# Performance work log

Measured on AMD Instinct MI355X. Metric: run time of the kernel, lower is better.

## Reference

```python
import jax, jax.numpy as jnp
import numpy as np
import math

D = 128
RATIO = 0.8
BN_EPS = 1e-5
N_NODES = 40000
N_EDGES = 640000
Y_SIZE = 8


def _prelu(x, a):
    return jnp.where(x > 0, x, a * x)


def setup_inputs() -> dict:
    key = jax.random.key(0)
    ks = jax.random.split(key, 16)
    inv = lambda n: 1.0 / np.sqrt(n)
    return {
        "x": jax.random.normal(ks[0], (N_NODES, 1), jnp.float32),
        "edge_index": jax.random.randint(ks[1], (2, N_EDGES), 0, N_NODES, jnp.int32),
        "W1": jax.random.normal(ks[2], (1, D), jnp.float32),
        "V1": jax.random.normal(ks[3], (1, D), jnp.float32),
        "Ws": jax.random.normal(ks[4], (9, D, D), jnp.float32) * inv(D),
        "Vs": jax.random.normal(ks[5], (9, D, D), jnp.float32) * inv(D),
        "conv_b": jax.random.normal(ks[6], (10, D), jnp.float32) * 0.01,
        "bn_gamma": 1.0 + 0.1 * jax.random.normal(ks[7], (10, D), jnp.float32),
        "bn_beta": 0.1 * jax.random.normal(ks[8], (10, D), jnp.float32),
        "bn_mean": jnp.zeros((10, D), jnp.float32),
        "bn_var": jnp.ones((10, D), jnp.float32),
        "pool_p": jax.random.normal(ks[9], (10, D), jnp.float32),
        "prelu_a": 0.25 * jnp.ones((1,), jnp.float32),
        "lin1_w": jax.random.normal(ks[10], (2560, 1280), jnp.float32) * inv(2560),
        "lin1_b": jax.random.normal(ks[11], (1280,), jnp.float32) * 0.01,
        "lin2_w": jax.random.normal(ks[12], (1280, Y_SIZE), jnp.float32) * inv(1280),
        "lin2_b": jax.random.normal(ks[13], (Y_SIZE,), jnp.float32) * 0.01,
    }


def reference(x, edge_index, W1, V1, Ws, Vs, conv_b, bn_gamma, bn_beta, bn_mean,
              bn_var, pool_p, prelu_a, lin1_w, lin1_b, lin2_w, lin2_b):
    # Single graph (batch all zeros). Edge array stays fixed size with a validity mask.
    src, dst = edge_index[0], edge_index[1]
    emask = jnp.ones(src.shape, dtype=bool)
    n = x.shape[0]
    h = x
    reads = []
    for i in range(10):
        W = W1 if i == 0 else Ws[i - 1]
        V = V1 if i == 0 else Vs[i - 1]
        # ---- ARMAConv (num_stacks=1, num_layers=1): relu(L_hat (h W) + h V + b)
        ew = emask.astype(h.dtype)
        deg = jax.ops.segment_sum(ew, dst, num_segments=n)
        dinv = jnp.where(deg > 0, 1.0 / jnp.sqrt(deg), 0.0)
        norm = dinv[dst] * dinv[src] * ew                      # [E]
        hw = h @ W                                             # [n, D]
        agg = jax.ops.segment_sum(hw[src] * norm[:, None], dst, num_segments=n)
        h = jax.nn.relu(agg + h @ V + conv_b[i])
        # ---- BatchNorm1d (eval mode, running stats)
        h = (h - bn_mean[i]) * (bn_gamma[i] / jnp.sqrt(bn_var[i] + BN_EPS)) + bn_beta[i]
        # ---- shared PReLU
        h = _prelu(h, prelu_a)
        # ---- TopKPooling(ratio=0.8): score = tanh(h.p/||p||), keep ceil(0.8n)
        p = pool_p[i]
        score = jnp.tanh(h @ p / jnp.linalg.norm(p))
        k = math.ceil(RATIO * n)
        topv, idx = jax.lax.top_k(score, k)
        h = h[idx] * topv[:, None]                             # [k, D]
        remap = jnp.full((n,), -1, jnp.int32).at[idx].set(jnp.arange(k, dtype=jnp.int32))
        ns, nd = remap[src], remap[dst]
        emask = emask & (ns >= 0) & (nd >= 0)
        src = jnp.where(emask, ns, 0)
        dst = jnp.where(emask, nd, 0)
        n = k
        # ---- global max + mean pool (single graph)
        reads.append(jnp.concatenate([h.max(axis=0), h.mean(axis=0)]))
    r = jnp.concatenate(reads)[None, :]                        # [1, 2560]
    z = _prelu(r @ lin1_w + lin1_b, prelu_a)                   # dropout = identity (eval)
    z = _prelu(z @ lin2_w + lin2_b, prelu_a)
    z = z - z.min(axis=1, keepdims=True)
    z = z / z.max(axis=1, keepdims=True)
    z = z / z.sum(axis=1, keepdims=True)
    return z
```

## Files before the change

kernel.cpp:

```cpp
#include <hip/hip_runtime.h>
#include <hip/hip_bf16.h>

#define NEDGE 640000
#define NMAX  40000
#define SB    40
#define PRB   256
#define EBLK  512
#define FB    1280
#define LIN1B 64
#define GRB   32
#define HTS   36
#define TKB   32
#define GHN   5632
#define GBMAX 2048

__device__ inline unsigned orderKey(float s) {
    unsigned b = __float_as_uint(s);
    return (b & 0x80000000u) ? ~b : (b | 0x80000000u);
}

__device__ inline void histAdd(int* sh, int bin, bool act, int nbits) {
    unsigned long long mm = __ballot(act);
    for (int b = 0; b < nbits; b++) {
        unsigned long long bal = __ballot(act && ((bin >> b) & 1));
        mm &= ((bin >> b) & 1) ? bal : ~bal;
    }
    if (act) {
        int lane = threadIdx.x & 63;
        int leader = __ffsll(mm) - 1;
        if (lane == leader) atomicAdd(&sh[bin], __popcll(mm));
    }
}

__device__ inline void gridbar(int* ctr, int target) {
    __syncthreads();
    if (threadIdx.x == 0) {
        __threadfence();
        __hip_atomic_fetch_add(ctr, 1, __ATOMIC_RELEASE, __HIP_MEMORY_SCOPE_AGENT);
        while (__hip_atomic_load(ctr, __ATOMIC_ACQUIRE, __HIP_MEMORY_SCOPE_AGENT) < target)
            __builtin_amdgcn_s_sleep(1);
        __threadfence();
    }
    __syncthreads();
}

__device__ inline void suffixSel2048(int* lh, const int* gh, int rem, int* outD, int* outR) {
    int t = threadIdx.x;
    lh[t] = gh[t]; lh[t+1024] = gh[t+1024];
    __syncthreads();
    for (int off = 1; off < 2048; off <<= 1) {
        int v0 = lh[t]      + ((t+off < 2048)      ? lh[t+off]      : 0);
        int v1 = lh[t+1024] + ((t+1024+off < 2048) ? lh[t+1024+off] : 0);
        __syncthreads();
        lh[t] = v0; lh[t+1024] = v1;
        __syncthreads();
    }
    for (int d = t; d < 2048; d += 1024) {
        int S = lh[d], Sn = (d == 2047) ? 0 : lh[d+1];
        if (S >= rem && Sn < rem) { *outD = d; *outR = rem - Sn; }
    }
    __syncthreads();
}

__device__ inline void suffixSel1024(int* lh, const int* gh, int rem, int* outD, int* outR) {
    int t = threadIdx.x;
    lh[t] = gh[t];
    __syncthreads();
    for (int off = 1; off < 1024; off <<= 1) {
        int v0 = lh[t] + ((t+off < 1024) ? lh[t+off] : 0);
        __syncthreads();
        lh[t] = v0;
        __syncthreads();
    }
    {
        int S = lh[t], Sn = (t == 1023) ? 0 : lh[t+1];
        if (S >= rem && Sn < rem) { *outD = t; *outR = rem - Sn; }
    }
    __syncthreads();
}

__device__ inline void prefixSel256(int* lh, const int* gh, int rem, int* outD, int* outR) {
    int t = threadIdx.x;
    if (t < 256) lh[t] = gh[t];
    __syncthreads();
    for (int off = 1; off < 256; off <<= 1) {
        int v = 0;
        if (t < 256) v = lh[t] + ((t >= off) ? lh[t-off] : 0);
        __syncthreads();
        if (t < 256) lh[t] = v;
        __syncthreads();
    }
    if (t < 256) {
        int P = lh[t], Pp = (t == 0) ? 0 : lh[t-1];
        if (P >= rem && Pp < rem) { *outD = t; *outR = rem - Pp; }
    }
    __syncthreads();
}

__device__ inline void poolReduceT(const float* __restrict__ scr, float* __restrict__ rbuf,
                                   int gbP, int L, int ch) {
    int t = threadIdx.x;
    bool isMax = ch < 128;
    float acc = isMax ? -3.402823e38f : 0.f;
    for (int r = t; r < gbP; r += 256) {
        float v = scr[(size_t)ch*GBMAX + r];
        acc = isMax ? fmaxf(acc, v) : (acc + v);
    }
    __shared__ float red[256];
    red[t] = acc; __syncthreads();
    for (int st = 128; st > 0; st >>= 1) {
        if (t < st) red[t] = isMax ? fmaxf(red[t], red[t+st]) : (red[t] + red[t+st]);
        __syncthreads();
    }
    if (t == 0) rbuf[L*256 + ch] = red[0];
}

__device__ const float c_invk[10] = {
    1.0f/32000.0f, 1.0f/25600.0f, 1.0f/20480.0f, 1.0f/16384.0f, 1.0f/13108.0f,
    1.0f/10487.0f, 1.0f/8390.0f,  1.0f/6712.0f,  1.0f/5370.0f,  1.0f/4296.0f };

__global__ void k_init(const int* __restrict__ eidx, int* __restrict__ esrc,
                       int* __restrict__ edst, int* __restrict__ erank,
                       const float* __restrict__ poolp,
                       float* __restrict__ rbuf, float* __restrict__ pnorm,
                       int* __restrict__ ecnt, int* __restrict__ degA,
                       int* __restrict__ tkc) {
    int b = blockIdx.x, t = threadIdx.x;
    if (b < 10) {
        rbuf[b*256 + t] = (t < 128) ? -3.402823e38f : 0.0f;
        __shared__ float red[256];
        float v = 0.0f;
        if (t < 128) { float pv = poolp[b*128 + t]; v = pv*pv; }
        red[t] = v; __syncthreads();
        for (int s = 128; s > 0; s >>= 1) { if (t < s) red[t] += red[t+s]; __syncthreads(); }
        if (t == 0) pnorm[b] = sqrtf(red[0]);
    }
    if (b == 10 && t < 16) ecnt[t] = (t == 0) ? NEDGE : 0;
    if (b == 11 && t < 64) tkc[t] = 0;
    int e = b*256 + t;
    if (e < NEDGE) {
        int d = eidx[NEDGE + e];
        esrc[e] = eidx[e]; edst[e] = d;
        erank[e] = atomicAdd(&degA[d], 1);
    }
}

__global__ __launch_bounds__(256) void k_presum(const int* __restrict__ deg,
                                                int* __restrict__ lbsum,
                                                int n, int chunk) {
    int b = blockIdx.x, t = threadIdx.x;
    __shared__ int red[256];
    int start = b*chunk, end = min(start + chunk, n);
    int s = 0;
    for (int i = start + t; i < end; i += 256) s += deg[i];
    red[t] = s; __syncthreads();
    for (int st = 128; st > 0; st >>= 1) { if (t < st) red[t] += red[t+st]; __syncthreads(); }
    if (t == 0) lbsum[b] = red[0];
}

__global__ void k_scan(const int* __restrict__ deg,
                       int* __restrict__ offs, float* __restrict__ dinv,
                       int* __restrict__ ghist, int* __restrict__ selbuf,
                       const int* __restrict__ lbsum,
                       const float* __restrict__ scr, float* __restrict__ rbuf,
                       int n, int chunk, int gbP, int prevL) {
    int b = blockIdx.x, t = threadIdx.x, lane = t & 63, wid = t >> 6;
    if (b >= SB) {
        if (gbP > 0) poolReduceT(scr, rbuf, gbP, prevL, b - SB);
        return;
    }
    __shared__ int s_excl;
    __shared__ int wsum[4];
    __shared__ int s_carry;
    __shared__ int s_sums[SB];
    if (b == 0) {
        for (int jj = t; jj < GHN; jj += 256) ghist[jj] = 0;
        if (t == 0) { selbuf[2] = 0; selbuf[5] = 0; }
    }
    if (t < SB) s_sums[t] = lbsum[t];
    __syncthreads();
    if (t == 0) {
        int excl = 0;
        for (int p = 0; p < b; p++) excl += s_sums[p];
        s_excl = excl;
    }
    __syncthreads();
    if (t == 0) s_carry = s_excl;
    __syncthreads();
    int start = b*chunk, end = min(start + chunk, n);
    for (int base = start; base < end; base += 256) {
        int i = base + t;
        int d = (i < end) ? deg[i] : 0;
        int incl = d;
        for (int off = 1; off < 64; off <<= 1) {
            int o = __shfl_up(incl, off);
            if (lane >= off) incl += o;
        }
        if (lane == 63) wsum[wid] = incl;
        __syncthreads();
        if (t == 0) { int c = s_carry; for (int w = 0; w < 4; w++) { int tmp = wsum[w]; wsum[w] = c; c += tmp; } s_carry = c; }
        __syncthreads();
        int p = wsum[wid] + incl - d;
        if (i < end) {
            offs[i] = p;
            dinv[i] = (d > 0) ? 1.0f/sqrtf((float)d) : 0.0f;
        }
        __syncthreads();
    }
}

__global__ __launch_bounds__(128) void k_fill(const int* __restrict__ esrc, const int* __restrict__ edst,
                                              const int* __restrict__ erank, const int* __restrict__ offs,
                                              int* __restrict__ csr, const int* __restrict__ ecnt) {
    int ec = *ecnt;
    for (int e = blockIdx.x*128 + threadIdx.x; e < ec; e += FB*128)
        csr[offs[edst[e]] + erank[e]] = esrc[e];
}

__global__ __launch_bounds__(128) void k_gather0(
    const float* __restrict__ x, const float* __restrict__ W1, const float* __restrict__ V1,
    const float* __restrict__ convb,
    const float* __restrict__ bng, const float* __restrict__ bnb,
    const float* __restrict__ bnm, const float* __restrict__ bnv,
    const float* __restrict__ poolp, const float* __restrict__ pnorm,
    const float* __restrict__ prelua,
    const int* __restrict__ offs, const int* __restrict__ deg, const float* __restrict__ dinv,
    const int* __restrict__ csr,
    float* __restrict__ AGG, float* __restrict__ score, unsigned* __restrict__ keys) {
    int v = blockIdx.x, j = threadIdx.x;
    __shared__ float red[128];
    int off = offs[v], dg = deg[v];
    float accs = 0.0f;
    for (int c = j; c < dg; c += 128) { int s = csr[off + c]; accs += x[s]*dinv[s]; }
    red[j] = accs; __syncthreads();
    for (int st = 64; st > 0; st >>= 1) { if (j < st) red[j] += red[j+st]; __syncthreads(); }
    float aggs = red[0] * dinv[v];
    __syncthreads();
    float h2 = aggs*W1[j] + x[v]*V1[j] + convb[j];
    h2 = fmaxf(h2, 0.0f);
    float scale = bng[j] / sqrtf(bnv[j] + 1e-5f);
    h2 = (h2 - bnm[j])*scale + bnb[j];
    float a = prelua[0];
    h2 = (h2 > 0.0f) ? h2 : a*h2;
    AGG[v*128 + j] = h2;
    red[j] = h2 * poolp[j]; __syncthreads();
    for (int st = 64; st > 0; st >>= 1) { if (j < st) red[j] += red[j+st]; __syncthreads(); }
    if (j == 0) {
        float sc = tanhf(red[0] / pnorm[0]);
        score[v] = sc;
        keys[v]  = orderKey(sc);
    }
}

__global__ __launch_bounds__(128) void k_gather(
    const float* __restrict__ HW, float* __restrict__ AGG,
    const int* __restrict__ offs, const int* __restrict__ deg, const float* __restrict__ dinv,
    const int* __restrict__ csr,
    const float* __restrict__ bng, const float* __restrict__ bnb,
    const float* __restrict__ bnm, const float* __restrict__ bnv,
    const float* __restrict__ poolp, const float* __restrict__ pnorm,
    const float* __restrict__ prelua,
    float* __restrict__ score, unsigned* __restrict__ keys, int layer) {
    int v = blockIdx.x, j = threadIdx.x;
    __shared__ int   s_src[128];
    __shared__ float s_dv[128];
    __shared__ float red[128];
    int off = offs[v], dg = deg[v];
    float acc = 0.0f;
    for (int base = 0; base < dg; base += 128) {
        int cnt = min(128, dg - base);
        if (j < cnt) { int s = csr[off + base + j]; s_src[j] = s; s_dv[j] = dinv[s]; }
        __syncthreads();
        for (int c = 0; c < cnt; c++) acc += HW[s_src[c]*128 + j] * s_dv[c];
        __syncthreads();
    }
    int gj = layer*128 + j;
    float h2 = AGG[v*128 + j] + acc*dinv[v];
    h2 = fmaxf(h2, 0.0f);
    float scale = bng[gj] / sqrtf(bnv[gj] + 1e-5f);
    h2 = (h2 - bnm[gj])*scale + bnb[gj];
    float a = prelua[0];
    h2 = (h2 > 0.0f) ? h2 : a*h2;
    AGG[v*128 + j] = h2;
    red[j] = h2 * poolp[gj]; __syncthreads();
    for (int st = 64; st > 0; st >>= 1) { if (j < st) red[j] += red[j+st]; __syncthreads(); }
    if (j == 0) {
        float sc = tanhf(red[0] / pnorm[layer]);
        score[v] = sc;
        keys[v]  = orderKey(sc);
    }
}

__global__ __launch_bounds__(1024) void k_topk(const unsigned* __restrict__ keys,
                                               int* __restrict__ gh, int* __restrict__ selbuf,
                                               int* __restrict__ degN,
                                               int* __restrict__ remap, int* __restrict__ keep_ids,
                                               int* __restrict__ bar, int n, int kk) {
    __shared__ int lh[2048];
    __shared__ int s_d1, s_r1, s_dA, s_rA, s_dB, s_ntk, s_bC, s_r2, s_lowD, s_lowR;
    __shared__ int s_base, s_cur;
    int t = threadIdx.x, b = blockIdx.x, lane = t & 63;
    int* h1 = gh;
    int* h2 = gh + 2048;
    int* h3 = gh + 4096;
    int* h4 = gh + 5120;
    int* h5 = gh + 5376;

    for (int i = b*1024 + t; i < NMAX; i += TKB*1024) degN[i] = 0;

    int nR = (n + 1023) & ~1023;
    lh[t] = 0; lh[t+1024] = 0;
    __syncthreads();
    for (int i = b*1024 + t; i < nR; i += TKB*1024) {
        bool act = (i < n);
        int bin = act ? (int)(keys[i] >> 21) : 0;
        histAdd(lh, bin, act, 11);
    }
    __syncthreads();
    { int c = lh[t]; if (c) atomicAdd(&h1[t], c); c = lh[t+1024]; if (c) atomicAdd(&h1[t+1024], c); }
    gridbar(&bar[0], TKB);
    suffixSel2048(lh, h1, kk, &s_d1, &s_r1);
    int bstar = s_d1;

    lh[t] = 0; lh[t+1024] = 0;
    __syncthreads();
    for (int i = b*1024 + t; i < nR; i += TKB*1024) {
        bool act = false; int bin = 0;
        if (i < n) { unsigned key = keys[i]; act = ((int)(key >> 21) == bstar); bin = (int)((key >> 10) & 2047); }
        histAdd(lh, act ? bin : 0, act, 11);
    }
    __syncthreads();
    { int c = lh[t]; if (c) atomicAdd(&h2[t], c); c = lh[t+1024]; if (c) atomicAdd(&h2[t+1024], c); }
    gridbar(&bar[1], TKB);
    suffixSel2048(lh, h2, s_r1, &s_dA, &s_rA);
    unsigned top21 = ((unsigned)bstar << 11) | (unsigned)s_dA;

    lh[t] = 0;
    __syncthreads();
    for (int i = b*1024 + t; i < nR; i += TKB*1024) {
        bool act = false; int bin = 0;
        if (i < n) { unsigned key = keys[i]; act = ((key >> 10) == top21); bin = (int)(key & 1023); }
        histAdd(lh, act ? bin : 0, act, 10);
    }
    __syncthreads();
    { int c = lh[t]; if (c) atomicAdd(&h3[t], c); }
    gridbar(&bar[2], TKB);
    suffixSel1024(lh, h3, s_rA, &s_dB, &s_ntk);
    unsigned thresh = (top21 << 10) | (unsigned)s_dB;

    if (t < 256) lh[t] = 0;
    __syncthreads();
    for (int i = b*1024 + t; i < n; i += TKB*1024)
        if (keys[i] == thresh) atomicAdd(&lh[i >> 8], 1);
    __syncthreads();
    if (t < 256) { int c = lh[t]; if (c) atomicAdd(&h4[t], c); }
    gridbar(&bar[3], TKB);
    prefixSel256(lh, h4, s_ntk, &s_bC, &s_r2);
    int bC = s_bC;

    if (t < 256) lh[t] = 0;
    __syncthreads();
    for (int i = b*1024 + t; i < n; i += TKB*1024)
        if (keys[i] == thresh && (i >> 8) == bC) atomicAdd(&lh[i & 255], 1);
    __syncthreads();
    if (t < 256) { int c = lh[t]; if (c) atomicAdd(&h5[t], c); }
    gridbar(&bar[4], TKB);
    prefixSel256(lh, h5, s_r2, &s_lowD, &s_lowR);
    int cut = (bC << 8) | s_lowD;

    {
        int cnt = 0;
        for (int base = b*1024; base < n; base += TKB*1024) {
            int i = base + t;
            if (i < n) {
                unsigned key = keys[i];
                cnt += (key > thresh) || (key == thresh && i <= cut);
            }
        }
        lh[t] = cnt; __syncthreads();
        for (int st = 512; st > 0; st >>= 1) { if (t < st) lh[t] += lh[t+st]; __syncthreads(); }
        if (t == 0) { s_base = atomicAdd(&selbuf[5], lh[0]); s_cur = 0; }
        __syncthreads();
        for (int base = b*1024; base < n; base += TKB*1024) {
            int i = base + t;
            bool keep = false;
            if (i < n) {
                unsigned key = keys[i];
                keep = (key > thresh) || (key == thresh && i <= cut);
            }
            unsigned long long m = __ballot(keep);
            int wcnt = __popcll(m);
            int wbase = 0;
            if (lane == 0 && wcnt) wbase = atomicAdd(&s_cur, wcnt);
            wbase = __shfl(wbase, 0);
            if (keep) {
                int slot = s_base + wbase + __popcll(m & ((1ULL << lane) - 1));
                remap[i] = slot; keep_ids[slot] = i;
            } else if (i < n) remap[i] = -1;
        }
    }
}

__global__ __launch_bounds__(128) void k_poolgemm(
        const float* __restrict__ AGGc, const float* __restrict__ score,
        const int* __restrict__ keep_ids, const int* __restrict__ remap,
        float* __restrict__ scr,
        const int* __restrict__ esrcP, const int* __restrict__ edstP,
        int* __restrict__ esrcN, int* __restrict__ edstN, int* __restrict__ erankN,
        const int* __restrict__ ecntP, int* __restrict__ ecntN, int* __restrict__ degN,
        const float* __restrict__ W, const float* __restrict__ V, const float* __restrict__ bias,
        float* __restrict__ HW, float* __restrict__ AGGn, int k, int gb, int do_gemm) {
    int b = blockIdx.x, t = threadIdx.x;
    __shared__ __align__(16) float ht[128*HTS];
    if (b < gb) {
        int v0 = b * GRB;
        float mx = -3.402823e38f, sm = 0.f;
        #pragma unroll
        for (int it = 0; it < GRB; it++) {
            int r = v0 + it;
            bool valid = (r < k);
            int vv = keep_ids[valid ? r : (k - 1)];
            float val = AGGc[(size_t)vv*128 + t] * score[vv];
            if (!valid) val = 0.f;
            ht[t*HTS + it] = val;
            if (valid) { mx = fmaxf(mx, val); sm += val; }
        }
        scr[(size_t)t*GBMAX + b]         = mx;
        scr[(size_t)(t+128)*GBMAX + b]   = sm;
        if (!do_gemm) return;
        __syncthreads();
        float accW[GRB], accV[GRB];
        #pragma unroll
        for (int r = 0; r < GRB; r++) { accW[r] = 0.0f; accV[r] = 0.0f; }
        #pragma unroll 4
        for (int kk = 0; kk < 128; kk++) {
            float mw = W[kk*128 + t];
            float mv = V[kk*128 + t];
            const float* hp = &ht[kk*HTS];
            #pragma unroll
            for (int r4 = 0; r4 < GRB; r4 += 4) {
                float4 hq = *(const float4*)(hp + r4);
                accW[r4+0] += hq.x*mw;  accV[r4+0] += hq.x*mv;
                accW[r4+1] += hq.y*mw;  accV[r4+1] += hq.y*mv;
                accW[r4+2] += hq.z*mw;  accV[r4+2] += hq.z*mv;
                accW[r4+3] += hq.w*mw;  accV[r4+3] += hq.w*mv;
            }
        }
        float bb = bias[t];
        for (int r = 0; r < GRB; r++) {
            int v = v0 + r;
            if (v >= k) break;
            HW[(size_t)v*128 + t]   = accW[r];
            AGGn[(size_t)v*128 + t] = accV[r] + bb;
        }
    } else {
        int eb = b - gb, lane = t & 63;
        int ec = *ecntP;
        int* red = (int*)ht;
        __shared__ int s_base, s_cur;
        int cnt = 0;
        for (int base = eb*128; base < ec; base += EBLK*128) {
            int e = base + t;
            if (e < ec) {
                int ns = remap[esrcP[e]], nd = remap[edstP[e]];
                cnt += (ns >= 0 && nd >= 0);
            }
        }
        red[t] = cnt; __syncthreads();
        for (int st = 64; st > 0; st >>= 1) { if (t < st) red[t] += red[t+st]; __syncthreads(); }
        if (t == 0) { s_base = atomicAdd(ecntN, red[0]); s_cur = 0; }
        __syncthreads();
        for (int base = eb*128; base < ec; base += EBLK*128) {
            int e = base + t;
            bool keep = false; int ns = 0, nd = 0;
            if (e < ec) {
                ns = remap[esrcP[e]]; nd = remap[edstP[e]];
                keep = (ns >= 0 && nd >= 0);
            }
            unsigned long long m = __ballot(keep);
            int wcnt = __popcll(m);
            int wbase = 0;
            if (lane == 0 && wcnt) wbase = atomicAdd(&s_cur, wcnt);
            wbase = __shfl(wbase, 0);
            if (keep) {
                int pos = s_base + wbase + __popcll(m & ((1ULL << lane) - 1));
                esrcN[pos] = ns; edstN[pos] = nd;
                erankN[pos] = atomicAdd(&degN[nd], 1);
            }
        }
    }
}

__global__ __launch_bounds__(256) void k_pred(const float* __restrict__ scr, float* __restrict__ rbuf,
                                              int gbP, int L) {
    poolReduceT(scr, rbuf, gbP, L, blockIdx.x);
}

__global__ __launch_bounds__(320) void k_lin1(const float* __restrict__ rbuf,
                                              const float* __restrict__ w1,
                                              float* __restrict__ z1part) {
    int b = blockIdx.x, t = threadIdx.x;
    int j = t*4;
    float4 acc = make_float4(0.f, 0.f, 0.f, 0.f);
    int i0 = b*40;
    for (int r = 0; r < 40; r++) {
        int i = i0 + r;
        float rv = rbuf[i];
        if (i & 128) rv *= c_invk[i >> 8];
        float4 w = *(const float4*)(w1 + (size_t)i*1280 + j);
        acc.x += rv*w.x; acc.y += rv*w.y; acc.z += rv*w.z; acc.w += rv*w.w;
    }
    *(float4*)(z1part + b*1280 + j) = acc;
}

__global__ __launch_bounds__(320) void k_lin2(const float* __restrict__ z1part,
                                              const float* __restrict__ b1,
                                              const float* __restrict__ w2, const float* __restrict__ b2,
                                              const float* __restrict__ prelua, float* __restrict__ out) {
    int t = threadIdx.x, lane = t & 63, wid = t >> 6;
    float a = prelua[0];
    int j = t*4;
    float4 acc = make_float4(0.f, 0.f, 0.f, 0.f);
    for (int p = 0; p < LIN1B; p++) {
        float4 v = *(const float4*)(z1part + p*1280 + j);
        acc.x += v.x; acc.y += v.y; acc.z += v.z; acc.w += v.w;
    }
    float4 bb = *(const float4*)(b1 + j);
    float z0 = acc.x + bb.x; z0 = z0 > 0.f ? z0 : a*z0;
    float z1 = acc.y + bb.y; z1 = z1 > 0.f ? z1 : a*z1;
    float z2 = acc.z + bb.z; z2 = z2 > 0.f ? z2 : a*z2;
    float z3 = acc.w + bb.w; z3 = z3 > 0.f ? z3 : a*z3;
    float s[8];
    #pragma unroll
    for (int o = 0; o < 8; o++)
        s[o] = z0*w2[(j+0)*8+o] + z1*w2[(j+1)*8+o] + z2*w2[(j+2)*8+o] + z3*w2[(j+3)*8+o];
    #pragma unroll
    for (int off = 32; off > 0; off >>= 1)
        #pragma unroll
        for (int o = 0; o < 8; o++) s[o] += __shfl_down(s[o], off);
    __shared__ float sred[5][8];
    if (lane == 0)
        for (int o = 0; o < 8; o++) sred[wid][o] = s[o];
    __syncthreads();
    if (t == 0) {
        float zo[8];
        for (int o = 0; o < 8; o++) {
            float z = sred[0][o]+sred[1][o]+sred[2][o]+sred[3][o]+sred[4][o] + b2[o];
            zo[o] = z > 0.f ? z : a*z;
        }
        float mn = zo[0];
        for (int o = 1; o < 8; o++) mn = fminf(mn, zo[o]);
        float v[8], mx = -3.402823e38f;
        for (int o = 0; o < 8; o++) { v[o] = zo[o] - mn; mx = fmaxf(mx, v[o]); }
        float sm = 0.f;
        for (int o = 0; o < 8; o++) { v[o] = v[o] / mx; sm += v[o]; }
        for (int o = 0; o < 8; o++) out[o] = v[o] / sm;
    }
}

extern "C" void kernel_launch(void* const* d_in, const int* in_sizes, int n_in,
                              void* d_out, int out_size, void* d_ws, size_t ws_size,
                              hipStream_t stream) {
    const float* x      = (const float*)d_in[0];
    const int*   eidx   = (const int*)  d_in[1];
    const float* W1     = (const float*)d_in[2];
    const float* V1     = (const float*)d_in[3];
    const float* Ws     = (const float*)d_in[4];
    const float* Vs     = (const float*)d_in[5];
    const float* convb  = (const float*)d_in[6];
    const float* bng    = (const float*)d_in[7];
    const float* bnb    = (const float*)d_in[8];
    const float* bnm    = (const float*)d_in[9];
    const float* bnv    = (const float*)d_in[10];
    const float* poolp  = (const float*)d_in[11];
    const float* prelua = (const float*)d_in[12];
    const float* w1     = (const float*)d_in[13];
    const float* b1     = (const float*)d_in[14];
    const float* w2     = (const float*)d_in[15];
    const float* b2     = (const float*)d_in[16];
    float* out = (float*)d_out;

    float* wsf  = (float*)d_ws;
    float* aggA   = wsf;
    float* aggB   = aggA  + (size_t)NMAX*128;
    float* HW     = aggB  + (size_t)NMAX*128;
    float* dinv   = HW    + (size_t)NMAX*128;
    float* score  = dinv  + NMAX;
    float* rbuf   = score + NMAX;
    float* pnorm  = rbuf  + 2560;
    float* z1part = pnorm + 16;
    float* scr    = z1part + LIN1B*1280;
    unsigned* keys = (unsigned*)(scr + (size_t)GBMAX*256);
    int* esrcA  = (int*)(keys + NMAX);
    int* edstA  = esrcA + NEDGE;
    int* erankA = edstA + NEDGE;
    int* esrcB  = erankA + NEDGE;
    int* edstB  = esrcB + NEDGE;
    int* erankB = edstB + NEDGE;
    int* csr    = erankB + NEDGE;
    int* degA   = csr   + NEDGE;
    int* degB   = degA  + NMAX;
    int* ghist  = degB  + NMAX;
    int* offs   = ghist + GHN;
    int* remap  = offs  + NMAX;
    int* keep_ids = remap + NMAX;
    int* lbsum  = keep_ids + NMAX;
    int* ecnt   = lbsum + SB*2;
    int* selbuf = ecnt  + 16;
    int* tkc    = selbuf + 16;

    static const int NS[10] = {40000,32000,25600,20480,16384,13108,10487,8390,6712,5370};
    static const int KS[10] = {32000,25600,20480,16384,13108,10487,8390,6712,5370,4296};

    hipMemsetAsync(degA, 0, (size_t)NMAX*sizeof(int), stream);
    k_init<<<2500, 256, 0, stream>>>(eidx, esrcA, edstA, erankA, poolp, rbuf, pnorm,
                                     ecnt, degA, tkc);

    for (int i = 0; i < 10; i++) {
        int n = NS[i], k = KS[i];
        int chunk = (n + SB - 1) / SB;
        int* esrcP  = (i & 1) ? esrcB  : esrcA;
        int* edstP  = (i & 1) ? edstB  : edstA;
        int* erankP = (i & 1) ? erankB : erankA;
        int* esrcN  = (i & 1) ? esrcA  : esrcB;
        int* edstN  = (i & 1) ? edstA  : edstB;
        int* erankN = (i & 1) ? erankA : erankB;
        int* degP   = (i & 1) ? degB : degA;
        int* degN   = (i & 1) ? degA : degB;
        float* AGGc = (i & 1) ? aggB : aggA;
        float* AGGn = (i & 1) ? aggA : aggB;

        int gbP = (i == 0) ? 0 : (KS[i-1] + GRB - 1) / GRB;
        k_presum<<<SB, 256, 0, stream>>>(degP, lbsum, n, chunk);
        k_scan<<<SB + PRB, 256, 0, stream>>>(degP, offs, dinv, ghist, selbuf,
                                             lbsum, scr, rbuf, n, chunk,
                                             gbP, i - 1);

        k_fill<<<FB, 128, 0, stream>>>(esrcP, edstP, erankP, offs, csr, &ecnt[i]);

        if (i == 0) {
            k_gather0<<<n, 128, 0, stream>>>(x, W1, V1, convb,
                                             bng, bnb, bnm, bnv, poolp, pnorm, prelua,
                                             offs, degP, dinv, csr, AGGc, score, keys);
        } else {
            k_gather<<<n, 128, 0, stream>>>(HW, AGGc, offs, degP, dinv, csr,
                                            bng, bnb, bnm, bnv, poolp, pnorm, prelua,
                                            score, keys, i);
        }

        k_topk<<<TKB, 1024, 0, stream>>>(keys, ghist, selbuf, degN,
                                         remap, keep_ids, tkc + i*5, n, k);

        int gb = (k + GRB - 1) / GRB;
        int do_gemm = (i < 9);
        int grid = gb + (do_gemm ? EBLK : 0);
        k_poolgemm<<<grid, 128, 0, stream>>>(AGGc, score, keep_ids, remap, scr,
                                             esrcP, edstP, esrcN, edstN, erankN,
                                             &ecnt[i], &ecnt[i+1], degN,
                                             Ws + (size_t)min(i,8)*16384,
                                             Vs + (size_t)min(i,8)*16384,
                                             convb + min(i+1,9)*128,
                                             HW, AGGn, k, gb, do_gemm);
    }

    k_pred<<<PRB, 256, 0, stream>>>(scr, rbuf, (KS[9] + GRB - 1) / GRB, 9);
    k_lin1<<<LIN1B, 320, 0, stream>>>(rbuf, w1, z1part);
    k_lin2<<<1, 320, 0, stream>>>(z1part, b1, w2, b2, prelua, out);
}
```

Measured before the change: 1.179 ms.

## Speed up top-k selection scans, skip tie-break passes, and shrink GEMM row tile

```diff
diff --git a/kernel.cpp b/kernel.cpp
--- a/kernel.cpp
+++ b/kernel.cpp
@@ -8,8 +8,8 @@
 #define EBLK  512
 #define FB    1280
 #define LIN1B 64
-#define GRB   32
-#define HTS   36
+#define GRB   16
+#define HTS   20
 #define TKB   32
 #define GHN   5632
 #define GBMAX 2048
@@ -44,38 +44,63 @@
     __syncthreads();
 }
 
-__device__ inline void suffixSel2048(int* lh, const int* gh, int rem, int* outD, int* outR) {
-    int t = threadIdx.x;
-    lh[t] = gh[t]; lh[t+1024] = gh[t+1024];
-    __syncthreads();
-    for (int off = 1; off < 2048; off <<= 1) {
-        int v0 = lh[t]      + ((t+off < 2048)      ? lh[t+off]      : 0);
-        int v1 = lh[t+1024] + ((t+1024+off < 2048) ? lh[t+1024+off] : 0);
-        __syncthreads();
-        lh[t] = v0; lh[t+1024] = v1;
-        __syncthreads();
-    }
-    for (int d = t; d < 2048; d += 1024) {
-        int S = lh[d], Sn = (d == 2047) ? 0 : lh[d+1];
-        if (S >= rem && Sn < rem) { *outD = d; *outR = rem - Sn; }
-    }
-    __syncthreads();
-}
-
-__device__ inline void suffixSel1024(int* lh, const int* gh, int rem, int* outD, int* outR) {
-    int t = threadIdx.x;
-    lh[t] = gh[t];
-    __syncthreads();
-    for (int off = 1; off < 1024; off <<= 1) {
-        int v0 = lh[t] + ((t+off < 1024) ? lh[t+off] : 0);
-        __syncthreads();
-        lh[t] = v0;
-        __syncthreads();
-    }
-    {
-        int S = lh[t], Sn = (t == 1023) ? 0 : lh[t+1];
-        if (S >= rem && Sn < rem) { *outD = t; *outR = rem - Sn; }
-    }
+__device__ inline int waveScanIncl(int v) {
+    int lane = threadIdx.x & 63;
+    #pragma unroll
+    for (int off = 1; off < 64; off <<= 1) {
+        int o = __shfl_up(v, off);
+        if (lane >= off) v += o;
+    }
+    return v;
+}
+
+__device__ inline void selScan2048(const int* gh, int rem, int* outD, int* outR, int* outCnt) {
+    __shared__ int wtot[16];
+    __shared__ int s_T;
+    int t = threadIdx.x, lane = t & 63, wid = t >> 6;
+    int a0 = gh[2*t], a1 = gh[2*t+1];
+    int s  = a0 + a1;
+    int ws = waveScanIncl(s);
+    if (lane == 63) wtot[wid] = ws;
+    __syncthreads();
+    if (t < 16) {
+        int v = wtot[t];
+        #pragma unroll
+        for (int off = 1; off < 16; off <<= 1) { int o = __shfl_up(v, off); if (lane >= off) v += o; }
+        wtot[t] = v;
+        if (t == 15) s_T = v;
+    }
+    __syncthreads();
+    int base = (wid > 0) ? wtot[wid-1] : 0;
+    int inclPair = base + ws;
+    int P1 = inclPair - a1;
+    int P0 = P1 - a0;
+    int Q = s_T - rem;
+    if (a0 > 0 && P0 <= Q && Q < P0 + a0) { *outD = 2*t;   *outR = a0 - (Q - P0); *outCnt = a0; }
+    if (a1 > 0 && P1 <= Q && Q < P1 + a1) { *outD = 2*t+1; *outR = a1 - (Q - P1); *outCnt = a1; }
+    __syncthreads();
+}
+
+__device__ inline void selScan1024(const int* gh, int rem, int* outD, int* outR, int* outCnt) {
+    __shared__ int wtot[16];
+    __shared__ int s_T;
+    int t = threadIdx.x, lane = t & 63, wid = t >> 6;
+    int a0 = gh[t];
+    int ws = waveScanIncl(a0);
+    if (lane == 63) wtot[wid] = ws;
+    __syncthreads();
+    if (t < 16) {
+        int v = wtot[t];
+        #pragma unroll
+        for (int off = 1; off < 16; off <<= 1) { int o = __shfl_up(v, off); if (lane >= off) v += o; }
+        wtot[t] = v;
+        if (t == 15) s_T = v;
+    }
+    __syncthreads();
+    int base = (wid > 0) ? wtot[wid-1] : 0;
+    int P0 = base + ws - a0;
+    int Q = s_T - rem;
+    if (a0 > 0 && P0 <= Q && Q < P0 + a0) { *outD = t; *outR = a0 - (Q - P0); *outCnt = a0; }
     __syncthreads();
 }
 
@@ -297,7 +322,7 @@
                                                int* __restrict__ remap, int* __restrict__ keep_ids,
                                                int* __restrict__ bar, int n, int kk) {
     __shared__ int lh[2048];
-    __shared__ int s_d1, s_r1, s_dA, s_rA, s_dB, s_ntk, s_bC, s_r2, s_lowD, s_lowR;
+    __shared__ int s_d1, s_r1, s_c1, s_dA, s_rA, s_cA, s_dB, s_ntk, s_cnt3, s_bC, s_r2, s_lowD, s_lowR;
     __shared__ int s_base, s_cur;
     int t = threadIdx.x, b = blockIdx.x, lane = t & 63;
     int* h1 = gh;
@@ -319,7 +344,7 @@
     __syncthreads();
     { int c = lh[t]; if (c) atomicAdd(&h1[t], c); c = lh[t+1024]; if (c) atomicAdd(&h1[t+1024], c); }
     gridbar(&bar[0], TKB);
-    suffixSel2048(lh, h1, kk, &s_d1, &s_r1);
+    selScan2048(h1, kk, &s_d1, &s_r1, &s_c1);
     int bstar = s_d1;
 
     lh[t] = 0; lh[t+1024] = 0;
@@ -332,7 +357,7 @@
     __syncthreads();
     { int c = lh[t]; if (c) atomicAdd(&h2[t], c); c = lh[t+1024]; if (c) atomicAdd(&h2[t+1024], c); }
     gridbar(&bar[1], TKB);
-    suffixSel2048(lh, h2, s_r1, &s_dA, &s_rA);
+    selScan2048(h2, s_r1, &s_dA, &s_rA, &s_cA);
     unsigned top21 = ((unsigned)bstar << 11) | (unsigned)s_dA;
 
     lh[t] = 0;
@@ -345,28 +370,33 @@
     __syncthreads();
     { int c = lh[t]; if (c) atomicAdd(&h3[t], c); }
     gridbar(&bar[2], TKB);
-    suffixSel1024(lh, h3, s_rA, &s_dB, &s_ntk);
+    selScan1024(h3, s_rA, &s_dB, &s_ntk, &s_cnt3);
     unsigned thresh = (top21 << 10) | (unsigned)s_dB;
 
-    if (t < 256) lh[t] = 0;
-    __syncthreads();
-    for (int i = b*1024 + t; i < n; i += TKB*1024)
-        if (keys[i] == thresh) atomicAdd(&lh[i >> 8], 1);
-    __syncthreads();
-    if (t < 256) { int c = lh[t]; if (c) atomicAdd(&h4[t], c); }
-    gridbar(&bar[3], TKB);
-    prefixSel256(lh, h4, s_ntk, &s_bC, &s_r2);
-    int bC = s_bC;
-
-    if (t < 256) lh[t] = 0;
-    __syncthreads();
-    for (int i = b*1024 + t; i < n; i += TKB*1024)
-        if (keys[i] == thresh && (i >> 8) == bC) atomicAdd(&lh[i & 255], 1);
-    __syncthreads();
-    if (t < 256) { int c = lh[t]; if (c) atomicAdd(&h5[t], c); }
-    gridbar(&bar[4], TKB);
-    prefixSel256(lh, h5, s_r2, &s_lowD, &s_lowR);
-    int cut = (bC << 8) | s_lowD;
+    int cut;
+    if (s_cnt3 == s_ntk) {
+        cut = n - 1;
+    } else {
+        if (t < 256) lh[t] = 0;
+        __syncthreads();
+        for (int i = b*1024 + t; i < n; i += TKB*1024)
+            if (keys[i] == thresh) atomicAdd(&lh[i >> 8], 1);
+        __syncthreads();
+        if (t < 256) { int c = lh[t]; if (c) atomicAdd(&h4[t], c); }
+        gridbar(&bar[3], TKB);
+        prefixSel256(lh, h4, s_ntk, &s_bC, &s_r2);
+        int bC = s_bC;
+
+        if (t < 256) lh[t] = 0;
+        __syncthreads();
+        for (int i = b*1024 + t; i < n; i += TKB*1024)
+            if (keys[i] == thresh && (i >> 8) == bC) atomicAdd(&lh[i & 255], 1);
+        __syncthreads();
+        if (t < 256) { int c = lh[t]; if (c) atomicAdd(&h5[t], c); }
+        gridbar(&bar[4], TKB);
+        prefixSel256(lh, h5, s_r2, &s_lowD, &s_lowR);
+        cut = (bC << 8) | s_lowD;
+    }
 
     {
         int cnt = 0;
@@ -425,28 +455,72 @@
             ht[t*HTS + it] = val;
             if (valid) { mx = fmaxf(mx, val); sm += val; }
         }
-        scr[(size_t)t*GBMAX + b]         = mx;
-        scr[(size_t)(t+128)*GBMAX + b]   = sm;
+        scr[(size_t)t*GBMAX + b]       = mx;
+        scr[(size_t)(t+128)*GBMAX + b] = sm;
         if (!do_gemm) return;
         __syncthreads();
         float accW[GRB], accV[GRB];
         #pragma unroll
         for (int r = 0; r < GRB; r++) { accW[r] = 0.0f; accV[r] = 0.0f; }
-        #pragma unroll 4
-        for (int kk = 0; kk < 128; kk++) {
-            float mw = W[kk*128 + t];
-            float mv = V[kk*128 + t];
-            const float* hp = &ht[kk*HTS];
-            #pragma unroll
-            for (int r4 = 0; r4 < GRB; r4 += 4) {
-                float4 hq = *(const float4*)(hp + r4);
-                accW[r4+0] += hq.x*mw;  accV[r4+0] += hq.x*mv;
-                accW[r4+1] += hq.y*mw;  accV[r4+1] += hq.y*mv;
-                accW[r4+2] += hq.z*mw;  accV[r4+2] += hq.z*mv;
-                accW[r4+3] += hq.w*mw;  accV[r4+3] += hq.w*mv;
-            }
+        const float* Wp = W + t;
+        const float* Vp = V + t;
+        float w0 = Wp[0],   w1 = Wp[128],   w2 = Wp[256],   w3 = Wp[384];
+        float y0 = Vp[0],   y1 = Vp[128],   y2 = Vp[256],   y3 = Vp[384];
+        for (int kk = 0; kk < 128; kk += 4) {
+            int nk = (kk + 4) & 127;
+            float nw0 = Wp[nk*128],       nw1 = Wp[nk*128 + 128];
+            float nw2 = Wp[nk*128 + 256], nw3 = Wp[nk*128 + 384];
+            float ny0 = Vp[nk*128],       ny1 = Vp[nk*128 + 128];
+            float ny2 = Vp[nk*128 + 256], ny3 = Vp[nk*128 + 384];
+            {
+                const float* hp = &ht[kk*HTS];
+                #pragma unroll
+                for (int r4 = 0; r4 < GRB; r4 += 4) {
+                    float4 hq = *(const float4*)(hp + r4);
+                    accW[r4+0] += hq.x*w0;  accV[r4+0] += hq.x*y0;
+                    accW[r4+1] += hq.y*w0;  accV[r4+1] += hq.y*y0;
+                    accW[r4+2] += hq.z*w0;  accV[r4+2] += hq.z*y0;
+                    accW[r4+3] += hq.w*w0;  accV[r4+3] += hq.w*y0;
+                }
+            }
+            {
+                const float* hp = &ht[(kk+1)*HTS];
+                #pragma unroll
+                for (int r4 = 0; r4 < GRB; r4 += 4) {
+                    float4 hq = *(const float4*)(hp + r4);
+                    accW[r4+0] += hq.x*w1;  accV[r4+0] += hq.x*y1;
+                    accW[r4+1] += hq.y*w1;  accV[r4+1] += hq.y*y1;
+                    accW[r4+2] += hq.z*w1;  accV[r4+2] += hq.z*y1;
+                    accW[r4+3] += hq.w*w1;  accV[r4+3] += hq.w*y1;
+                }
+            }
+            {
+                const float* hp = &ht[(kk+2)*HTS];
+                #pragma unroll
+                for (int r4 = 0; r4 < GRB; r4 += 4) {
+                    float4 hq = *(const float4*)(hp + r4);
+                    accW[r4+0] += hq.x*w2;  accV[r4+0] += hq.x*y2;
+                    accW[r4+1] += hq.y*w2;  accV[r4+1] += hq.y*y2;
+                    accW[r4+2] += hq.z*w2;  accV[r4+2] += hq.z*y2;
+                    accW[r4+3] += hq.w*w2;  accV[r4+3] += hq.w*y2;
+                }
+            }
+            {
+                const float* hp = &ht[(kk+3)*HTS];
+                #pragma unroll
+                for (int r4 = 0; r4 < GRB; r4 += 4) {
+                    float4 hq = *(const float4*)(hp + r4);
+                    accW[r4+0] += hq.x*w3;  accV[r4+0] += hq.x*y3;
+                    accW[r4+1] += hq.y*w3;  accV[r4+1] += hq.y*y3;
+                    accW[r4+2] += hq.z*w3;  accV[r4+2] += hq.z*y3;
+                    accW[r4+3] += hq.w*w3;  accV[r4+3] += hq.w*y3;
+                }
+            }
+            w0 = nw0; w1 = nw1; w2 = nw2; w3 = nw3;
+            y0 = ny0; y1 = ny1; y2 = ny2; y3 = ny3;
         }
         float bb = bias[t];
+        #pragma unroll
         for (int r = 0; r < GRB; r++) {
             int v = v0 + r;
             if (v >= k) break;
```

After: 1.095 ms. -7.1%, faster.
